# Performance work log

Measured on AMD Instinct MI355X. Metric: run time of the kernel, lower is better.

## Reference

```python
import jax, jax.numpy as jnp
import numpy as np

N_RELS = 3
MAX_COMPS = 128
EMBED_DIM = 256
BATCH = 64
SEQ_LEN = 2048


def setup_inputs() -> dict:
    key = jax.random.key(0)
    k1, k2, k3 = jax.random.split(key, 3)
    embds = jax.random.normal(k1, (BATCH, SEQ_LEN, EMBED_DIM), dtype=jnp.float32)
    # sparse component-selection mask; p=0.04 -> ~82 components/sample (< MAX_COMPS-1)
    choice_mask = jax.random.bernoulli(k2, 0.04, (BATCH, SEQ_LEN)).astype(jnp.int32)
    # hk.Linear(n_rels*embed_dim, with_bias=False): W [embed_dim, n_rels*embed_dim]
    W = jax.random.normal(k3, (EMBED_DIM, N_RELS * EMBED_DIM), dtype=jnp.float32) / np.sqrt(EMBED_DIM).astype(np.float32)
    return {"embds": embds, "choice_mask": choice_mask, "W": W}


def _single(embds, mask, W):
    """One sample: gather selected embeddings, pad, project, pairwise relation scores.
    embds: [S, D], mask: [S] int, W: [D, D*R]. Returns [M, M, R]."""
    M, D, R = MAX_COMPS, EMBED_DIM, N_RELS
    # stable sort moves selected positions to the front, preserving order
    order = jnp.argsort(-mask)                      # [S]
    gathered = embds[order[: M - 1]]                # [M-1, D]
    n = jnp.minimum(jnp.sum(mask), M - 1)           # number of real components
    valid = jnp.arange(M - 1) < n                   # [M-1]
    comps = jnp.where(valid[:, None], gathered, jnp.zeros((), embds.dtype))
    # root component = row of ones (pad constant_values=1 at the front in the original)
    from_embds = jnp.concatenate([jnp.ones((1, D), embds.dtype), comps], axis=0)  # [M, D]
    to_embds = (from_embds @ W).reshape(M, D, R)    # [M, D, R]
    # jnp.dot([M,D], [M,D,R]) contracts D -> [M, M, R]
    log_energies = jnp.einsum('id,jdr->ijr', from_embds, to_embds)
    # no links FROM the root component (index 0)
    log_energies = log_energies.at[0].set(-jnp.inf)
    pad_mask = jnp.concatenate([jnp.ones((1,), bool), valid])   # [M]
    available = pad_mask[:, None] & pad_mask[None, :]           # [M, M]
    return jnp.where(available[:, :, None], log_energies, -jnp.inf)


def reference(embds, choice_mask, W):
    return jax.vmap(lambda e, m: _single(e, m, W))(embds, choice_mask)
```

## Files before the change

kernel.cpp:

```cpp
#include <hip/hip_runtime.h>
#include <math.h>

#define BATCH 64
#define SEQ   2048
#define DIM   256
#define NREL  3
#define MC    128
#define MV    127
#define NCOL  (DIM*NREL)
#define OUTC  (MC*NREL)

#define NEG_SENTINEL (-3.0e38f)

typedef __attribute__((ext_vector_type(8))) short short8;
typedef __attribute__((ext_vector_type(4))) float floatx4;
typedef __attribute__((ext_vector_type(4))) unsigned short us4;
typedef __attribute__((ext_vector_type(8))) unsigned short us8;

__device__ __forceinline__ unsigned short f2bf(float f) {
  unsigned int u = __builtin_bit_cast(unsigned int, f);
  unsigned int r = u + 0x7FFFu + ((u >> 16) & 1u);
  return (unsigned short)(r >> 16);
}

__global__ __launch_bounds__(256) void k_scan(const int* __restrict__ mask,
                                              int* __restrict__ sel_ws,
                                              int* __restrict__ n_ws) {
  int b = blockIdx.x, t = threadIdx.x;
  __shared__ int s_cnt[256];
  const int* m = mask + (size_t)b * SEQ;
  int base = t * 8;
  int vals[8];
  int c = 0;
#pragma unroll
  for (int k = 0; k < 8; k++) { vals[k] = m[base + k]; c += (vals[k] != 0); }
  s_cnt[t] = c;
  __syncthreads();
  for (int off = 1; off < 256; off <<= 1) {
    int add = (t >= off) ? s_cnt[t - off] : 0;
    __syncthreads();
    s_cnt[t] += add;
    __syncthreads();
  }
  int incl = s_cnt[t];
  int excl = incl - c;
  int total = s_cnt[255];
  int* sel = sel_ws + b * MV;
  int rank = excl;
#pragma unroll
  for (int k = 0; k < 8; k++) {
    if (vals[k]) { if (rank < MV) sel[rank] = base + k; rank++; }
  }
  if (t == 0) n_ws[b] = (total < MV) ? total : MV;
}

__global__ __launch_bounds__(256) void k_build(const float* __restrict__ embds,
                                               const int* __restrict__ sel_ws,
                                               const int* __restrict__ n_ws,
                                               unsigned short* __restrict__ fwb) {
  int b = blockIdx.x;
  int n = n_ws[b];
  const int* sel = sel_ws + b * MV;
  int t = threadIdx.x;
  int rsub = t >> 6;
  int c4 = (t & 63) * 4;
#pragma unroll
  for (int p = 0; p < 4; p++) {
    int i = blockIdx.y * 16 + p * 4 + rsub;
    float4 v = make_float4(0.f, 0.f, 0.f, 0.f);
    if (i == 0) {
      v = make_float4(1.f, 1.f, 1.f, 1.f);
    } else if (i - 1 < n) {
      v = *(const float4*)(embds + ((size_t)b * SEQ + sel[i - 1]) * DIM + c4);
    }
    us4 o; o.x = f2bf(v.x); o.y = f2bf(v.y); o.z = f2bf(v.z); o.w = f2bf(v.w);
    *(us4*)(fwb + ((size_t)b * MC + i) * DIM + c4) = o;
  }
}

__global__ __launch_bounds__(256) void k_wconv(const float* __restrict__ W,
                                               unsigned short* __restrict__ Wt) {
  int idx = blockIdx.x * 256 + threadIdx.x;
  int nn = idx >> 3;
  int k0 = (idx & 7) * 32;
  unsigned short tmp[32];
#pragma unroll
  for (int e = 0; e < 32; e++) tmp[e] = f2bf(W[(size_t)(k0 + e) * NCOL + nn]);
#pragma unroll
  for (int q = 0; q < 4; q++)
    *(us8*)(Wt + (size_t)nn * DIM + k0 + q * 8) = *(us8*)&tmp[q * 8];
}

#define LDP 40
__global__ __launch_bounds__(256) void k_gemm1(const unsigned short* __restrict__ fwb,
                                               const unsigned short* __restrict__ Wt,
                                               unsigned short* __restrict__ to_b) {
  int b = blockIdx.y;
  int n0 = blockIdx.x * 128;
  const unsigned short* A = fwb + (size_t)b * MC * DIM;
  const unsigned short* Bt = Wt + (size_t)n0 * DIM;
  __shared__ unsigned short As[128 * LDP];
  __shared__ unsigned short Bs[128 * LDP];
  int t = threadIdx.x;
  int wave = t >> 6, l = t & 63;
  int wr = wave >> 1, wc = wave & 1;
  int lm = l & 15, lk = (l >> 4) * 8;
  floatx4 acc[4][4] = {};
  for (int k0 = 0; k0 < DIM; k0 += 32) {
#pragma unroll
    for (int p = 0; p < 2; p++) {
      int idx = p * 256 + t;
      int row = idx >> 2, seg = (idx & 3) * 8;
      *(us8*)(&As[row * LDP + seg]) = *(const us8*)(A + (size_t)row * DIM + k0 + seg);
      *(us8*)(&Bs[row * LDP + seg]) = *(const us8*)(Bt + (size_t)row * DIM + k0 + seg);
    }
    __syncthreads();
    short8 af[4], bf[4];
#pragma unroll
    for (int mi = 0; mi < 4; mi++)
      af[mi] = *(short8*)&As[(wr * 64 + mi * 16 + lm) * LDP + lk];
#pragma unroll
    for (int ni = 0; ni < 4; ni++)
      bf[ni] = *(short8*)&Bs[(wc * 64 + ni * 16 + lm) * LDP + lk];
#pragma unroll
    for (int mi = 0; mi < 4; mi++)
#pragma unroll
      for (int ni = 0; ni < 4; ni++)
        acc[mi][ni] = __builtin_amdgcn_mfma_f32_16x16x32_bf16(af[mi], bf[ni], acc[mi][ni], 0, 0, 0);
    __syncthreads();
  }
  int rb = (l >> 4) * 4;
#pragma unroll
  for (int mi = 0; mi < 4; mi++)
#pragma unroll
    for (int ni = 0; ni < 4; ni++) {
      int ng = n0 + wc * 64 + ni * 16 + lm;
#pragma unroll
      for (int reg = 0; reg < 4; reg++) {
        int j = wr * 64 + mi * 16 + rb + reg;
        to_b[(size_t)b * MC * NCOL + (size_t)j * NCOL + ng] = f2bf(acc[mi][ni][reg]);
      }
    }
}

__global__ __launch_bounds__(256) void k_rel(const unsigned short* __restrict__ fwb,
                                             const unsigned short* __restrict__ to_b,
                                             const int* __restrict__ n_ws,
                                             float* __restrict__ out) {
  int b = blockIdx.y;
  int bc = blockIdx.x;
  int j0 = bc * 32, c0 = bc * 96;
  const unsigned short* A = fwb + (size_t)b * MC * DIM;
  const unsigned short* T = to_b + (size_t)b * MC * NCOL;
  __shared__ unsigned short As[128 * LDP];
  __shared__ unsigned short Bs[96 * LDP];
  int t = threadIdx.x;
  int w = t >> 6, l = t & 63;
  int lm = l & 15, lk = (l >> 4) * 8;
  floatx4 acc[2][6] = {};
  int jl = t >> 3;
  int l8 = t & 7;
  for (int k0 = 0; k0 < DIM; k0 += 32) {
#pragma unroll
    for (int p = 0; p < 2; p++) {
      int idx = p * 256 + t;
      int row = idx >> 2, seg = (idx & 3) * 8;
      *(us8*)(&As[row * LDP + seg]) = *(const us8*)(A + (size_t)row * DIM + k0 + seg);
    }
    {
      const unsigned short* src = T + (size_t)(j0 + jl) * NCOL + 3 * k0 + l8 * 12;
      us4 q0 = *(const us4*)(src);
      us4 q1 = *(const us4*)(src + 4);
      us4 q2 = *(const us4*)(src + 8);
      unsigned short vv[12] = { q0.x, q0.y, q0.z, q0.w, q1.x, q1.y, q1.z, q1.w,
                                q2.x, q2.y, q2.z, q2.w };
#pragma unroll
      for (int e = 0; e < 12; e++) {
        int q = l8 * 12 + e;
        Bs[(jl * 3 + (q % 3)) * LDP + (q / 3)] = vv[e];
      }
    }
    __syncthreads();
    short8 af[2], bf[6];
#pragma unroll
    for (int mi = 0; mi < 2; mi++)
      af[mi] = *(short8*)&As[(w * 32 + mi * 16 + lm) * LDP + lk];
#pragma unroll
    for (int ci = 0; ci < 6; ci++)
      bf[ci] = *(short8*)&Bs[(ci * 16 + lm) * LDP + lk];
#pragma unroll
    for (int mi = 0; mi < 2; mi++)
#pragma unroll
      for (int ci = 0; ci < 6; ci++)
        acc[mi][ci] = __builtin_amdgcn_mfma_f32_16x16x32_bf16(af[mi], bf[ci], acc[mi][ci], 0, 0, 0);
    __syncthreads();
  }
  int n = n_ws[b];
  int rb = (l >> 4) * 4;
#pragma unroll
  for (int mi = 0; mi < 2; mi++)
#pragma unroll
    for (int ci = 0; ci < 6; ci++) {
      int cg = c0 + ci * 16 + lm;
      int j = cg / 3;
      bool vj = (j == 0) || (j <= n);
#pragma unroll
      for (int reg = 0; reg < 4; reg++) {
        int i = w * 32 + mi * 16 + rb + reg;
        bool vi = (i > 0) && (i <= n);
        out[(size_t)b * MC * OUTC + (size_t)i * OUTC + cg] =
            (vi && vj) ? acc[mi][ci][reg] : NEG_SENTINEL;
      }
    }
}

extern "C" void kernel_launch(void* const* d_in, const int* in_sizes, int n_in,
                              void* d_out, int out_size, void* d_ws, size_t ws_size,
                              hipStream_t stream) {
  const float* embds = (const float*)d_in[0];
  const int*   mask  = (const int*)d_in[1];
  const float* W     = (const float*)d_in[2];
  float* out = (float*)d_out;

  char* ws = (char*)d_ws;
  int* n_ws   = (int*)(ws + 0);
  int* sel_ws = (int*)(ws + 1024);
  unsigned short* fwb  = (unsigned short*)(ws + 65536);
  unsigned short* Wt   = (unsigned short*)(ws + 65536 + 4*1024*1024);
  unsigned short* to_b = (unsigned short*)(ws + 65536 + 5*1024*1024);

  k_scan <<<dim3(BATCH),      dim3(256), 0, stream>>>(mask, sel_ws, n_ws);
  k_build<<<dim3(BATCH, 8),   dim3(256), 0, stream>>>(embds, sel_ws, n_ws, fwb);
  k_wconv<<<dim3(24),         dim3(256), 0, stream>>>(W, Wt);
  k_gemm1<<<dim3(6, BATCH),   dim3(256), 0, stream>>>(fwb, Wt, to_b);
  k_rel  <<<dim3(4, BATCH),   dim3(256), 0, stream>>>(fwb, to_b, n_ws, out);
}
```

Measured before the change: 199.6 us.

## Fuse scan and gather kernels, drop LDS staging in GEMMs

New measurement: 202.0 us. About the same (+1.2%).

```diff
diff --git a/kernel.cpp b/kernel.cpp
--- a/kernel.cpp
+++ b/kernel.cpp
@@ -23,58 +23,63 @@
   return (unsigned short)(r >> 16);
 }
 
-__global__ __launch_bounds__(256) void k_scan(const int* __restrict__ mask,
-                                              int* __restrict__ sel_ws,
+__global__ __launch_bounds__(256) void k_prep(const int* __restrict__ mask,
+                                              const float* __restrict__ embds,
+                                              unsigned short* __restrict__ fwb,
                                               int* __restrict__ n_ws) {
   int b = blockIdx.x, t = threadIdx.x;
-  __shared__ int s_cnt[256];
+  int lane = t & 63, wv = t >> 6;
+  __shared__ int sel[MV];
+  __shared__ int wsum[4];
   const int* m = mask + (size_t)b * SEQ;
   int base = t * 8;
   int vals[8];
   int c = 0;
 #pragma unroll
   for (int k = 0; k < 8; k++) { vals[k] = m[base + k]; c += (vals[k] != 0); }
-  s_cnt[t] = c;
+  int inc = c;
+#pragma unroll
+  for (int off = 1; off < 64; off <<= 1) {
+    int o = __shfl_up(inc, off, 64);
+    if (lane >= off) inc += o;
+  }
+  if (lane == 63) wsum[wv] = inc;
   __syncthreads();
-  for (int off = 1; off < 256; off <<= 1) {
-    int add = (t >= off) ? s_cnt[t - off] : 0;
-    __syncthreads();
-    s_cnt[t] += add;
-    __syncthreads();
-  }
-  int incl = s_cnt[t];
-  int excl = incl - c;
-  int total = s_cnt[255];
-  int* sel = sel_ws + b * MV;
+  int wbase = 0;
+#pragma unroll
+  for (int w = 0; w < 4; w++) if (w < wv) wbase += wsum[w];
+  int total = wsum[0] + wsum[1] + wsum[2] + wsum[3];
+  int excl = wbase + inc - c;
   int rank = excl;
 #pragma unroll
   for (int k = 0; k < 8; k++) {
     if (vals[k]) { if (rank < MV) sel[rank] = base + k; rank++; }
   }
-  if (t == 0) n_ws[b] = (total < MV) ? total : MV;
-}
-
-__global__ __launch_bounds__(256) void k_build(const float* __restrict__ embds,
-                                               const int* __restrict__ sel_ws,
-                                               const int* __restrict__ n_ws,
-                                               unsigned short* __restrict__ fwb) {
-  int b = blockIdx.x;
-  int n = n_ws[b];
-  const int* sel = sel_ws + b * MV;
-  int t = threadIdx.x;
-  int rsub = t >> 6;
-  int c4 = (t & 63) * 4;
-#pragma unroll
-  for (int p = 0; p < 4; p++) {
-    int i = blockIdx.y * 16 + p * 4 + rsub;
-    float4 v = make_float4(0.f, 0.f, 0.f, 0.f);
+  int n = (total < MV) ? total : MV;
+  if (t == 0) n_ws[b] = n;
+  __syncthreads();
+  int lane16 = t & 15;
+#pragma unroll
+  for (int p = 0; p < 8; p++) {
+    int i = p * 16 + (t >> 4);
+    float f[16];
     if (i == 0) {
-      v = make_float4(1.f, 1.f, 1.f, 1.f);
+#pragma unroll
+      for (int e = 0; e < 16; e++) f[e] = 1.f;
     } else if (i - 1 < n) {
-      v = *(const float4*)(embds + ((size_t)b * SEQ + sel[i - 1]) * DIM + c4);
-    }
-    us4 o; o.x = f2bf(v.x); o.y = f2bf(v.y); o.z = f2bf(v.z); o.w = f2bf(v.w);
-    *(us4*)(fwb + ((size_t)b * MC + i) * DIM + c4) = o;
+      const float* src = embds + ((size_t)b * SEQ + sel[i - 1]) * DIM + lane16 * 16;
+#pragma unroll
+      for (int q = 0; q < 4; q++) *(float4*)&f[q * 4] = *(const float4*)(src + q * 4);
+    } else {
+#pragma unroll
+      for (int e = 0; e < 16; e++) f[e] = 0.f;
+    }
+    us8 o0, o1;
+#pragma unroll
+    for (int e = 0; e < 8; e++) { o0[e] = f2bf(f[e]); o1[e] = f2bf(f[8 + e]); }
+    unsigned short* dst = fwb + ((size_t)b * MC + i) * DIM + lane16 * 16;
+    *(us8*)(dst) = o0;
+    *(us8*)(dst + 8) = o1;
   }
 }
 
@@ -91,43 +96,31 @@
     *(us8*)(Wt + (size_t)nn * DIM + k0 + q * 8) = *(us8*)&tmp[q * 8];
 }
 
-#define LDP 40
 __global__ __launch_bounds__(256) void k_gemm1(const unsigned short* __restrict__ fwb,
                                                const unsigned short* __restrict__ Wt,
                                                unsigned short* __restrict__ to_b) {
   int b = blockIdx.y;
   int n0 = blockIdx.x * 128;
   const unsigned short* A = fwb + (size_t)b * MC * DIM;
-  const unsigned short* Bt = Wt + (size_t)n0 * DIM;
-  __shared__ unsigned short As[128 * LDP];
-  __shared__ unsigned short Bs[128 * LDP];
   int t = threadIdx.x;
   int wave = t >> 6, l = t & 63;
   int wr = wave >> 1, wc = wave & 1;
   int lm = l & 15, lk = (l >> 4) * 8;
   floatx4 acc[4][4] = {};
+#pragma unroll 2
   for (int k0 = 0; k0 < DIM; k0 += 32) {
-#pragma unroll
-    for (int p = 0; p < 2; p++) {
-      int idx = p * 256 + t;
-      int row = idx >> 2, seg = (idx & 3) * 8;
-      *(us8*)(&As[row * LDP + seg]) = *(const us8*)(A + (size_t)row * DIM + k0 + seg);
-      *(us8*)(&Bs[row * LDP + seg]) = *(const us8*)(Bt + (size_t)row * DIM + k0 + seg);
-    }
-    __syncthreads();
     short8 af[4], bf[4];
 #pragma unroll
     for (int mi = 0; mi < 4; mi++)
-      af[mi] = *(short8*)&As[(wr * 64 + mi * 16 + lm) * LDP + lk];
+      af[mi] = *(const short8*)(A + (size_t)(wr * 64 + mi * 16 + lm) * DIM + k0 + lk);
 #pragma unroll
     for (int ni = 0; ni < 4; ni++)
-      bf[ni] = *(short8*)&Bs[(wc * 64 + ni * 16 + lm) * LDP + lk];
+      bf[ni] = *(const short8*)(Wt + (size_t)(n0 + wc * 64 + ni * 16 + lm) * DIM + k0 + lk);
 #pragma unroll
     for (int mi = 0; mi < 4; mi++)
 #pragma unroll
       for (int ni = 0; ni < 4; ni++)
         acc[mi][ni] = __builtin_amdgcn_mfma_f32_16x16x32_bf16(af[mi], bf[ni], acc[mi][ni], 0, 0, 0);
-    __syncthreads();
   }
   int rb = (l >> 4) * 4;
 #pragma unroll
@@ -143,6 +136,7 @@
     }
 }
 
+#define LDB 264
 __global__ __launch_bounds__(256) void k_rel(const unsigned short* __restrict__ fwb,
                                              const unsigned short* __restrict__ to_b,
                                              const int* __restrict__ n_ws,
@@ -152,48 +146,42 @@
   int j0 = bc * 32, c0 = bc * 96;
   const unsigned short* A = fwb + (size_t)b * MC * DIM;
   const unsigned short* T = to_b + (size_t)b * MC * NCOL;
-  __shared__ unsigned short As[128 * LDP];
-  __shared__ unsigned short Bs[96 * LDP];
+  __shared__ unsigned short Bs[96 * LDB];
   int t = threadIdx.x;
   int w = t >> 6, l = t & 63;
   int lm = l & 15, lk = (l >> 4) * 8;
-  floatx4 acc[2][6] = {};
   int jl = t >> 3;
   int l8 = t & 7;
+#pragma unroll
+  for (int ch = 0; ch < 8; ch++) {
+    const unsigned short* src = T + (size_t)(j0 + jl) * NCOL + ch * 96 + l8 * 12;
+    us4 q0 = *(const us4*)(src);
+    us4 q1 = *(const us4*)(src + 4);
+    us4 q2 = *(const us4*)(src + 8);
+    unsigned short vv[12] = { q0.x, q0.y, q0.z, q0.w, q1.x, q1.y, q1.z, q1.w,
+                              q2.x, q2.y, q2.z, q2.w };
+#pragma unroll
+    for (int e = 0; e < 12; e++) {
+      int q = l8 * 12 + e;
+      Bs[(jl * 3 + (q % 3)) * LDB + ch * 32 + (q / 3)] = vv[e];
+    }
+  }
+  __syncthreads();
+  floatx4 acc[2][6] = {};
+#pragma unroll 2
   for (int k0 = 0; k0 < DIM; k0 += 32) {
-#pragma unroll
-    for (int p = 0; p < 2; p++) {
-      int idx = p * 256 + t;
-      int row = idx >> 2, seg = (idx & 3) * 8;
-      *(us8*)(&As[row * LDP + seg]) = *(const us8*)(A + (size_t)row * DIM + k0 + seg);
-    }
-    {
-      const unsigned short* src = T + (size_t)(j0 + jl) * NCOL + 3 * k0 + l8 * 12;
-      us4 q0 = *(const us4*)(src);
-      us4 q1 = *(const us4*)(src + 4);
-      us4 q2 = *(const us4*)(src + 8);
-      unsigned short vv[12] = { q0.x, q0.y, q0.z, q0.w, q1.x, q1.y, q1.z, q1.w,
-                                q2.x, q2.y, q2.z, q2.w };
-#pragma unroll
-      for (int e = 0; e < 12; e++) {
-        int q = l8 * 12 + e;
-        Bs[(jl * 3 + (q % 3)) * LDP + (q / 3)] = vv[e];
-      }
-    }
-    __syncthreads();
     short8 af[2], bf[6];
 #pragma unroll
     for (int mi = 0; mi < 2; mi++)
-      af[mi] = *(short8*)&As[(w * 32 + mi * 16 + lm) * LDP + lk];
+      af[mi] = *(const short8*)(A + (size_t)(w * 32 + mi * 16 + lm) * DIM + k0 + lk);
 #pragma unroll
     for (int ci = 0; ci < 6; ci++)
-      bf[ci] = *(short8*)&Bs[(ci * 16 + lm) * LDP + lk];
+      bf[ci] = *(const short8*)&Bs[(ci * 16 + lm) * LDB + k0 + lk];
 #pragma unroll
     for (int mi = 0; mi < 2; mi++)
 #pragma unroll
       for (int ci = 0; ci < 6; ci++)
         acc[mi][ci] = __builtin_amdgcn_mfma_f32_16x16x32_bf16(af[mi], bf[ci], acc[mi][ci], 0, 0, 0);
-    __syncthreads();
   }
   int n = n_ws[b];
   int rb = (l >> 4) * 4;
@@ -223,15 +211,13 @@
   float* out = (float*)d_out;
 
   char* ws = (char*)d_ws;
-  int* n_ws   = (int*)(ws + 0);
-  int* sel_ws = (int*)(ws + 1024);
+  int* n_ws = (int*)(ws + 0);
   unsigned short* fwb  = (unsigned short*)(ws + 65536);
   unsigned short* Wt   = (unsigned short*)(ws + 65536 + 4*1024*1024);
   unsigned short* to_b = (unsigned short*)(ws + 65536 + 5*1024*1024);
 
-  k_scan <<<dim3(BATCH),      dim3(256), 0, stream>>>(mask, sel_ws, n_ws);
-  k_build<<<dim3(BATCH, 8),   dim3(256), 0, stream>>>(embds, sel_ws, n_ws, fwb);
-  k_wconv<<<dim3(24),         dim3(256), 0, stream>>>(W, Wt);
-  k_gemm1<<<dim3(6, BATCH),   dim3(256), 0, stream>>>(fwb, Wt, to_b);
-  k_rel  <<<dim3(4, BATCH),   dim3(256), 0, stream>>>(fwb, to_b, n_ws, out);
-}
+  k_wconv<<<dim3(24),       dim3(256), 0, stream>>>(W, Wt);
+  k_prep <<<dim3(BATCH),    dim3(256), 0, stream>>>(mask, embds, fwb, n_ws);
+  k_gemm1<<<dim3(6, BATCH), dim3(256), 0, stream>>>(fwb, Wt, to_b);
+  k_rel  <<<dim3(4, BATCH), dim3(256), 0, stream>>>(fwb, to_b, n_ws, out);
+}
```
